# Performance work log

Hardware: AMD Instinct MI355X
Metric: run time of the kernel (lower is better)

Reference implementation:

```python
import jax, jax.numpy as jnp
import numpy as np

B, S, D = 4, 4096, 256


def setup_inputs() -> dict:
    key = jax.random.key(0)
    k1, k2, k3 = jax.random.split(key, 3)
    x = jax.random.normal(k1, (B, S, D), dtype=jnp.float32)
    w_int = jax.random.randint(k2, (D, D), 0, 127, dtype=jnp.int32)  # quantized weight (out, in)
    scale = jax.random.uniform(k3, (D,), dtype=jnp.float32)          # per-output-channel scale
    return {"x": x, "w_int": w_int, "scale": scale}


def reference(x, w_int, scale):
    # self-attention: q = k = v = x, single head over feature dim D
    inv_sqrt_d = 1.0 / jnp.sqrt(jnp.asarray(D, dtype=x.dtype))
    scores = jnp.einsum('bqd,bkd->bqk', x, x) * inv_sqrt_d   # [B,S,S]
    probs = jax.nn.softmax(scores, axis=-1)
    attn = jnp.einsum('bqk,bkd->bqd', probs, x)              # [B,S,D]
    # quantized linear: dequantize then matmul (y = attn @ W^T)
    W = w_int.astype(x.dtype) * scale[:, None]               # [D_out, D_in]
    return jnp.einsum('bsd,od->bso', attn, W)
```

## Files before the change

### kernel.cpp

```cpp
#include <hip/hip_runtime.h>

typedef __bf16 bf16x8 __attribute__((ext_vector_type(8)));
typedef float f32x16 __attribute__((ext_vector_type(16)));
typedef unsigned short u16x8 __attribute__((ext_vector_type(8)));

constexpr int B = 4, S = 4096, D = 256;
constexpr float CSC = 0.09016844005556021f;

static __device__ __forceinline__ unsigned short f2bf(float f) {
  unsigned int u = __builtin_bit_cast(unsigned int, f);
  u = (u + 0x7fffu + ((u >> 16) & 1u)) >> 16;
  return (unsigned short)u;
}

static __device__ __forceinline__ float bf2f(unsigned short u) {
  unsigned int v = ((unsigned int)u) << 16;
  return __builtin_bit_cast(float, v);
}

static __device__ __forceinline__ unsigned int pk2bf(float lo, float hi) {
  unsigned int r;
  asm("v_cvt_pk_bf16_f32 %0, %1, %2" : "=v"(r) : "v"(lo), "v"(hi));
  return r;
}

static __device__ __forceinline__ void gld16(const void* g, void* l) {
  __builtin_amdgcn_global_load_lds(
      (const __attribute__((address_space(1))) unsigned int*)g,
      (__attribute__((address_space(3))) unsigned int*)l, 16, 0, 0);
}

#define FENCE_ALL()                                               \
  do {                                                            \
    asm volatile("s_waitcnt vmcnt(0) lgkmcnt(0)" ::: "memory");   \
    __builtin_amdgcn_s_barrier();                                 \
    asm volatile("" ::: "memory");                                \
  } while (0)

__global__ __launch_bounds__(256) void k_prep(const float* __restrict__ x,
                                              unsigned short* __restrict__ xbf,
                                              unsigned short* __restrict__ xK,
                                              unsigned short* __restrict__ xV) {
  __shared__ unsigned short T[64][72];
  __shared__ unsigned short R[64][72];
  int bid = blockIdx.x;
  int b = bid >> 8, rem = bid & 255;
  int s0 = (rem >> 2) * 64, d0 = (rem & 3) * 64;
  int j = threadIdx.x & 63, i0 = threadIdx.x >> 6;
#pragma unroll
  for (int k = 0; k < 16; ++k) {
    int i = k * 4 + i0;
    int idx = (b * S + s0 + i) * D + d0 + j;
    unsigned short v = f2bf(x[idx]);
    xbf[idx] = v;
    T[j][i] = v;
    R[i][j] = v;
  }
  __syncthreads();
  int t = s0 >> 6;
#pragma unroll
  for (int p = 0; p < 2; ++p) {
    int cc = p * 256 + threadIdx.x;
    int i = cc >> 3;
    int sl = (cc >> 1) & 3;
    int half = cc & 1;
    u16x8 v = *(const u16x8*)&R[i][sl * 16 + half * 8];
    int s = (d0 >> 4) + sl;
    *(u16x8*)((char*)xK + (size_t)((b * 64 + t) * 16 + s) * 2048 + i * 32 + half * 16) = v;
  }
#pragma unroll
  for (int p = 0; p < 2; ++p) {
    int cc = p * 256 + threadIdx.x;
    int dl = cc >> 3;
    int p8 = cc & 7;
    u16x8 v = *(const u16x8*)&T[dl][p8 * 8];
    int c = p8 >> 1;
    *(u16x8*)((char*)xV + (size_t)((b * 64 + t) * 4 + c) * 8192 + (d0 + dl) * 32 +
              (p8 & 1) * 16) = v;
  }
}

__global__ __launch_bounds__(256) void k_deqw(const int* __restrict__ w,
                                              unsigned short* __restrict__ wbf) {
  int i = blockIdx.x * 256 + threadIdx.x;
  wbf[i] = f2bf((float)w[i]);
}

__global__ __launch_bounds__(512, 2) void k_attn(const unsigned short* __restrict__ xbf,
                                                 const unsigned short* __restrict__ xK,
                                                 const unsigned short* __restrict__ xV,
                                                 unsigned short* __restrict__ PO0,
                                                 unsigned short* __restrict__ PO1,
                                                 float* __restrict__ ML) {
  __shared__ __align__(16) char smem[132096];

  int tid = threadIdx.x;
  int w = tid >> 6, lane = tid & 63;
  int q5 = lane & 31, hi = lane >> 5;
  int pair = w >> 1, dh = w & 1;

  int bid = blockIdx.x;
  int swz = (bid & 7) * 32 + (bid >> 3);
  int h = swz & 1;
  int qg = swz >> 1;
  int q0 = qg * 128;
  int bat = q0 >> 12;
  int qloc = q0 & (S - 1);

  const unsigned short* Xb = xbf + (size_t)bat * (S * D);
  int qw = qloc + pair * 32;
  int koff = q5 * 32 + hi * 16;

  bf16x8 qf[16];
#pragma unroll
  for (int s = 0; s < 16; ++s)
    qf[s] = *(const bf16x8*)(Xb + (qw + q5) * D + s * 16 + hi * 8);

  f32x16 acc[8];
#pragma unroll
  for (int dt = 0; dt < 8; ++dt)
#pragma unroll
    for (int j = 0; j < 16; ++j) acc[dt][j] = 0.f;
  float l_lane = 0.f;

  const char* xKb = (const char*)xK + (size_t)(bat * 64 + h * 32) * 32768;
  const char* xVb = (const char*)xV + (size_t)(bat * 64 + h * 32) * 32768;

  auto STAGE = [&](int itile, int bb) {
    char* Kd = smem + bb * 32768;
    char* Vd = smem + 65536 + bb * 32768;
    const char* srcK = xKb + (size_t)itile * 32768;
    const char* srcV = xVb + (size_t)itile * 32768;
#pragma unroll
    for (int i = 0; i < 4; ++i) {
      int off = (w * 2 + (i >> 1)) * 2048 + (i & 1) * 1024;
      gld16(srcK + off + lane * 16, Kd + off);
    }
#pragma unroll
    for (int i = 0; i < 4; ++i) {
      int off = (w >> 1) * 8192 + ((w & 1) * 4 + i) * 1024;
      gld16(srcV + off + lane * 16, Vd + off);
    }
  };

  STAGE(0, 0);
  FENCE_ALL();

  for (int it = 0; it < 32; ++it) {
    int bb = it & 1;
    if (it + 1 < 32) STAGE(it + 1, bb ^ 1);

    const char* Kt = smem + bb * 32768 + dh * 1024 + koff;
    f32x16 st;
#pragma unroll
    for (int j = 0; j < 16; ++j) st[j] = 0.f;
    __builtin_amdgcn_s_setprio(1);
#pragma unroll
    for (int s = 0; s < 16; ++s) {
      bf16x8 kf = *(const bf16x8*)(Kt + s * 2048);
      st = __builtin_amdgcn_mfma_f32_32x32x16_bf16(kf, qf[s], st, 0, 0, 0);
    }
    __builtin_amdgcn_s_setprio(0);

    unsigned int pk[8];
    float ps = 0.f;
#pragma unroll
    for (int a = 0; a < 8; ++a) {
      float lo = exp2f(st[2 * a] * CSC);
      float hh = exp2f(st[2 * a + 1] * CSC);
      ps += lo + hh;
      pk[a] = pk2bf(lo, hh);
    }
    l_lane += ps;

    unsigned int a0 = pk[0], b0 = pk[2];
    unsigned int a1 = pk[1], b1 = pk[3];
    unsigned int a2 = pk[4], b2 = pk[6];
    unsigned int a3 = pk[5], b3 = pk[7];
    asm volatile("v_permlane32_swap_b32 %0, %1" : "+v"(a0), "+v"(b0));
    asm volatile("v_permlane32_swap_b32 %0, %1" : "+v"(a1), "+v"(b1));
    asm volatile("v_permlane32_swap_b32 %0, %1" : "+v"(a2), "+v"(b2));
    asm volatile("v_permlane32_swap_b32 %0, %1" : "+v"(a3), "+v"(b3));
    union PA { unsigned int u[4]; bf16x8 v; };
    PA pa0, pa1;
    pa0.u[0] = a0; pa0.u[1] = a1; pa0.u[2] = b0; pa0.u[3] = b1;
    pa1.u[0] = a2; pa1.u[1] = a3; pa1.u[2] = b2; pa1.u[3] = b3;

    __builtin_amdgcn_s_setprio(1);
#pragma unroll
    for (int s2i = 0; s2i < 2; ++s2i) {
      const char* Vt = smem + 65536 + bb * 32768 + (dh * 2 + s2i) * 8192 + koff;
      bf16x8 pa = (s2i == 0) ? pa0.v : pa1.v;
#pragma unroll
      for (int dt = 0; dt < 8; ++dt) {
        bf16x8 vf = *(const bf16x8*)(Vt + dt * 1024);
        acc[dt] = __builtin_amdgcn_mfma_f32_32x32x16_bf16(vf, pa, acc[dt], 0, 0, 0);
      }
    }
    __builtin_amdgcn_s_setprio(0);

    FENCE_ALL();
  }

  float lw = l_lane + __shfl_xor(l_lane, 32, 64);
  float* LX = (float*)(smem + 131072);
  if (lane < 32) LX[w * 32 + q5] = lw;
  __syncthreads();
  float l_tot = lw + LX[(w ^ 1) * 32 + q5];
  if (dh == 0 && lane < 32) {
    int row = q0 + pair * 32 + q5;
    ML[((size_t)h * 16384 + row) * 2 + 0] = 0.f;
    ML[((size_t)h * 16384 + row) * 2 + 1] = l_tot;
  }
  __syncthreads();

  unsigned short* Pb2 = (h == 0) ? PO0 : PO1;
#pragma unroll
  for (int rh = 0; rh < 2; ++rh) {
    float* slot = (float*)(smem + w * 16384);
#pragma unroll
    for (int dt4 = 0; dt4 < 4; ++dt4) {
#pragma unroll
      for (int r = 0; r < 16; ++r) {
        int dloc = dt4 * 32 + (r & 3) + 8 * (r >> 2) + 4 * hi;
        slot[dloc * 32 + q5] = acc[rh * 4 + dt4][r];
      }
    }
    __syncthreads();
    if (dh == rh) {
      const float* pslot = (const float*)(smem + (w ^ 1) * 16384);
#pragma unroll
      for (int dt4 = 0; dt4 < 4; ++dt4) {
#pragma unroll
        for (int r = 0; r < 16; ++r) {
          int dloc = dt4 * 32 + (r & 3) + 8 * (r >> 2) + 4 * hi;
          acc[rh * 4 + dt4][r] += pslot[dloc * 32 + q5];
        }
      }
      char* E = smem + w * 16384;
#pragma unroll
      for (int dt4 = 0; dt4 < 4; ++dt4) {
#pragma unroll
        for (int a = 0; a < 4; ++a) {
          int dl = dt4 * 32 + 8 * a + 4 * hi;
          *(unsigned int*)(E + q5 * 272 + dl * 2) =
              pk2bf(acc[rh * 4 + dt4][4 * a + 0], acc[rh * 4 + dt4][4 * a + 1]);
          *(unsigned int*)(E + q5 * 272 + dl * 2 + 4) =
              pk2bf(acc[rh * 4 + dt4][4 * a + 2], acc[rh * 4 + dt4][4 * a + 3]);
        }
      }
      asm volatile("s_waitcnt lgkmcnt(0)" ::: "memory");
#pragma unroll
      for (int i = 0; i < 8; ++i) {
        int qr = i * 4 + (lane >> 4);
        int ch = lane & 15;
        u16x8 v = *(const u16x8*)(E + qr * 272 + ch * 16);
        *(u16x8*)(Pb2 + (size_t)(q0 + pair * 32 + qr) * 256 + rh * 128 + ch * 8) = v;
      }
    }
    __syncthreads();
  }
}

__global__ __launch_bounds__(64) void k_gemm(const unsigned short* __restrict__ PO0,
                                             const unsigned short* __restrict__ PO1,
                                             const float* __restrict__ ML,
                                             const unsigned short* __restrict__ wbf,
                                             const float* __restrict__ scale,
                                             float* __restrict__ out) {
  int lane = threadIdx.x, g = lane >> 4, c = lane & 15;
  int m0 = blockIdx.x * 16;
  int o0 = blockIdx.y * 64;
  int row = m0 + c;
  float il = 1.f / (ML[(size_t)row * 2 + 1] + ML[((size_t)16384 + row) * 2 + 1]);
  union UU { uint4 u; bf16x8 v; };
  bf16x8 af[8];
#pragma unroll
  for (int dk = 0; dk < 8; ++dk) {
    u16x8 a0 = *(const u16x8*)(PO0 + (size_t)row * 256 + dk * 32 + g * 8);
    u16x8 a1 = *(const u16x8*)(PO1 + (size_t)row * 256 + dk * 32 + g * 8);
    UU cv;
#pragma unroll
    for (int e = 0; e < 4; ++e) {
      float lo = (bf2f(a0[2 * e]) + bf2f(a1[2 * e])) * il;
      float hi = (bf2f(a0[2 * e + 1]) + bf2f(a1[2 * e + 1])) * il;
      ((unsigned int*)&cv.u)[e] = pk2bf(lo, hi);
    }
    af[dk] = cv.v;
  }
  typedef float f32x4 __attribute__((ext_vector_type(4)));
  const f32x4 zero = {0.f, 0.f, 0.f, 0.f};
  f32x4 acc[4];
#pragma unroll
  for (int i = 0; i < 4; ++i) acc[i] = zero;
#pragma unroll
  for (int oc = 0; oc < 4; ++oc) {
#pragma unroll
    for (int dk = 0; dk < 8; ++dk) {
      bf16x8 wf = *(const bf16x8*)(wbf + (o0 + oc * 16 + c) * D + dk * 32 + g * 8);
      acc[oc] = __builtin_amdgcn_mfma_f32_16x16x32_bf16(af[dk], wf, acc[oc], 0, 0, 0);
    }
  }
#pragma unroll
  for (int oc = 0; oc < 4; ++oc) {
    float sc = scale[o0 + oc * 16 + c];
#pragma unroll
    for (int r = 0; r < 4; ++r)
      out[(m0 + 4 * g + r) * D + o0 + oc * 16 + c] = acc[oc][r] * sc;
  }
}

extern "C" void kernel_launch(void* const* d_in, const int* in_sizes, int n_in,
                              void* d_out, int out_size, void* d_ws, size_t ws_size,
                              hipStream_t stream) {
  (void)in_sizes; (void)n_in; (void)out_size; (void)ws_size;
  const float* x = (const float*)d_in[0];
  const int* w_int = (const int*)d_in[1];
  const float* scale = (const float*)d_in[2];
  float* out = (float*)d_out;

  char* ws = (char*)d_ws;
  unsigned short* xbf = (unsigned short*)(ws);
  unsigned short* xK  = (unsigned short*)(ws + 8388608);
  unsigned short* xV  = (unsigned short*)(ws + 16777216);
  unsigned short* wbf = (unsigned short*)(ws + 25165824);
  float*          ML  = (float*)(ws + 25296896);
  unsigned short* PO0 = (unsigned short*)(ws + 25821184);
  unsigned short* PO1 = (unsigned short*)(ws + 34209792);

  k_prep<<<dim3(1024), dim3(256), 0, stream>>>(x, xbf, xK, xV);
  k_deqw<<<dim3(256), dim3(256), 0, stream>>>(w_int, wbf);
  k_attn<<<dim3(256), dim3(512), 0, stream>>>(xbf, xK, xV, PO0, PO1, ML);
  k_gemm<<<dim3(1024, 4), dim3(64), 0, stream>>>(PO0, PO1, ML, wbf, scale, out);
}
```

Before: 116.7 us.

## Split QK MFMA chain into two accumulators and restructure output GEMM with LDS weights

In the attention kernel, the QK^T MFMA chain is split into two independent accumulators that are summed afterwards, which shortens the serial dependency between consecutive MFMAs. The output projection is rewritten so each 512-thread block handles 64 rows. It stages the whole bf16 weight matrix in LDS, in a layout pre-arranged by the dequant kernel, and uses 32x32x16 MFMAs. This replaces the 4096 tiny 64-thread blocks that reread weights from global memory, at the cost of 128KB of LDS per block and more vector registers.

```diff
diff --git a/kernel.cpp b/kernel.cpp
--- a/kernel.cpp
+++ b/kernel.cpp
@@ -81,9 +81,10 @@
 }
 
 __global__ __launch_bounds__(256) void k_deqw(const int* __restrict__ w,
-                                              unsigned short* __restrict__ wbf) {
-  int i = blockIdx.x * 256 + threadIdx.x;
-  wbf[i] = f2bf((float)w[i]);
+                                              unsigned short* __restrict__ wK) {
+  int o = blockIdx.x, d = threadIdx.x;
+  unsigned short v = f2bf((float)w[o * 256 + d]);
+  wK[(d >> 4) * 4096 + o * 16 + (d & 15)] = v;
 }
 
 __global__ __launch_bounds__(512, 2) void k_attn(const unsigned short* __restrict__ xbf,
@@ -151,16 +152,19 @@
     if (it + 1 < 32) STAGE(it + 1, bb ^ 1);
 
     const char* Kt = smem + bb * 32768 + dh * 1024 + koff;
-    f32x16 st;
-#pragma unroll
-    for (int j = 0; j < 16; ++j) st[j] = 0.f;
+    f32x16 sa, sb;
+#pragma unroll
+    for (int j = 0; j < 16; ++j) { sa[j] = 0.f; sb[j] = 0.f; }
     __builtin_amdgcn_s_setprio(1);
 #pragma unroll
-    for (int s = 0; s < 16; ++s) {
-      bf16x8 kf = *(const bf16x8*)(Kt + s * 2048);
-      st = __builtin_amdgcn_mfma_f32_32x32x16_bf16(kf, qf[s], st, 0, 0, 0);
+    for (int s = 0; s < 16; s += 2) {
+      bf16x8 kfa = *(const bf16x8*)(Kt + s * 2048);
+      bf16x8 kfb = *(const bf16x8*)(Kt + (s + 1) * 2048);
+      sa = __builtin_amdgcn_mfma_f32_32x32x16_bf16(kfa, qf[s], sa, 0, 0, 0);
+      sb = __builtin_amdgcn_mfma_f32_32x32x16_bf16(kfb, qf[s + 1], sb, 0, 0, 0);
     }
     __builtin_amdgcn_s_setprio(0);
+    f32x16 st = sa + sb;
 
     unsigned int pk[8];
     float ps = 0.f;
@@ -262,51 +266,71 @@
   }
 }
 
-__global__ __launch_bounds__(64) void k_gemm(const unsigned short* __restrict__ PO0,
-                                             const unsigned short* __restrict__ PO1,
-                                             const float* __restrict__ ML,
-                                             const unsigned short* __restrict__ wbf,
-                                             const float* __restrict__ scale,
-                                             float* __restrict__ out) {
-  int lane = threadIdx.x, g = lane >> 4, c = lane & 15;
-  int m0 = blockIdx.x * 16;
-  int o0 = blockIdx.y * 64;
-  int row = m0 + c;
+__global__ __launch_bounds__(512, 2) void k_gemm(const unsigned short* __restrict__ PO0,
+                                                 const unsigned short* __restrict__ PO1,
+                                                 const float* __restrict__ ML,
+                                                 const unsigned short* __restrict__ wK,
+                                                 const float* __restrict__ scale,
+                                                 float* __restrict__ out) {
+  __shared__ __align__(16) char Wl[131072];
+  int tid = threadIdx.x;
+  int w = tid >> 6, lane = tid & 63;
+  int q5 = lane & 31, hi = lane >> 5;
+  int msub = w & 1, oq = w >> 1;
+  int m0 = blockIdx.x * 64;
+
+#pragma unroll
+  for (int i = 0; i < 16; ++i) {
+    int off = (i * 512 + tid) * 16;
+    gld16((const char*)wK + off, Wl + off);
+  }
+
+  int row = m0 + msub * 32 + q5;
   float il = 1.f / (ML[(size_t)row * 2 + 1] + ML[((size_t)16384 + row) * 2 + 1]);
-  union UU { uint4 u; bf16x8 v; };
-  bf16x8 af[8];
-#pragma unroll
-  for (int dk = 0; dk < 8; ++dk) {
-    u16x8 a0 = *(const u16x8*)(PO0 + (size_t)row * 256 + dk * 32 + g * 8);
-    u16x8 a1 = *(const u16x8*)(PO1 + (size_t)row * 256 + dk * 32 + g * 8);
-    UU cv;
+
+  bf16x8 af[16];
+#pragma unroll
+  for (int s = 0; s < 16; ++s) {
+    u16x8 a0 = *(const u16x8*)(PO0 + (size_t)row * 256 + s * 16 + hi * 8);
+    u16x8 a1 = *(const u16x8*)(PO1 + (size_t)row * 256 + s * 16 + hi * 8);
+    union { unsigned int u[4]; bf16x8 v; } cv;
 #pragma unroll
     for (int e = 0; e < 4; ++e) {
       float lo = (bf2f(a0[2 * e]) + bf2f(a1[2 * e])) * il;
-      float hi = (bf2f(a0[2 * e + 1]) + bf2f(a1[2 * e + 1])) * il;
-      ((unsigned int*)&cv.u)[e] = pk2bf(lo, hi);
-    }
-    af[dk] = cv.v;
-  }
-  typedef float f32x4 __attribute__((ext_vector_type(4)));
-  const f32x4 zero = {0.f, 0.f, 0.f, 0.f};
-  f32x4 acc[4];
-#pragma unroll
-  for (int i = 0; i < 4; ++i) acc[i] = zero;
-#pragma unroll
-  for (int oc = 0; oc < 4; ++oc) {
-#pragma unroll
-    for (int dk = 0; dk < 8; ++dk) {
-      bf16x8 wf = *(const bf16x8*)(wbf + (o0 + oc * 16 + c) * D + dk * 32 + g * 8);
-      acc[oc] = __builtin_amdgcn_mfma_f32_16x16x32_bf16(af[dk], wf, acc[oc], 0, 0, 0);
-    }
-  }
-#pragma unroll
-  for (int oc = 0; oc < 4; ++oc) {
-    float sc = scale[o0 + oc * 16 + c];
-#pragma unroll
-    for (int r = 0; r < 4; ++r)
-      out[(m0 + 4 * g + r) * D + o0 + oc * 16 + c] = acc[oc][r] * sc;
+      float hh = (bf2f(a0[2 * e + 1]) + bf2f(a1[2 * e + 1])) * il;
+      cv.u[e] = pk2bf(lo, hh);
+    }
+    af[s] = cv.v;
+  }
+
+  asm volatile("s_waitcnt vmcnt(0)" ::: "memory");
+  __builtin_amdgcn_s_barrier();
+
+  f32x16 acc[2];
+#pragma unroll
+  for (int t = 0; t < 2; ++t)
+#pragma unroll
+    for (int j = 0; j < 16; ++j) acc[t][j] = 0.f;
+
+#pragma unroll
+  for (int t = 0; t < 2; ++t) {
+    int obase = (oq * 2 + t) * 32;
+#pragma unroll
+    for (int s = 0; s < 16; ++s) {
+      bf16x8 wf = *(const bf16x8*)(Wl + s * 8192 + (obase + q5) * 32 + hi * 16);
+      acc[t] = __builtin_amdgcn_mfma_f32_32x32x16_bf16(af[s], wf, acc[t], 0, 0, 0);
+    }
+  }
+
+#pragma unroll
+  for (int t = 0; t < 2; ++t) {
+    int o = (oq * 2 + t) * 32 + q5;
+    float sc = scale[o];
+#pragma unroll
+    for (int r = 0; r < 16; ++r) {
+      int mr = m0 + msub * 32 + (r & 3) + 8 * (r >> 2) + 4 * hi;
+      out[(size_t)mr * 256 + o] = acc[t][r] * sc;
+    }
   }
 }
 
@@ -323,13 +347,13 @@
   unsigned short* xbf = (unsigned short*)(ws);
   unsigned short* xK  = (unsigned short*)(ws + 8388608);
   unsigned short* xV  = (unsigned short*)(ws + 16777216);
-  unsigned short* wbf = (unsigned short*)(ws + 25165824);
+  unsigned short* wK  = (unsigned short*)(ws + 25165824);
   float*          ML  = (float*)(ws + 25296896);
   unsigned short* PO0 = (unsigned short*)(ws + 25821184);
   unsigned short* PO1 = (unsigned short*)(ws + 34209792);
 
   k_prep<<<dim3(1024), dim3(256), 0, stream>>>(x, xbf, xK, xV);
-  k_deqw<<<dim3(256), dim3(256), 0, stream>>>(w_int, wbf);
+  k_deqw<<<dim3(256), dim3(256), 0, stream>>>(w_int, wK);
   k_attn<<<dim3(256), dim3(512), 0, stream>>>(xbf, xK, xV, PO0, PO1, ML);
-  k_gemm<<<dim3(1024, 4), dim3(64), 0, stream>>>(PO0, PO1, ML, wbf, scale, out);
-}
+  k_gemm<<<dim3(256), dim3(512), 0, stream>>>(PO0, PO1, ML, wK, scale, out);
+}
```

Result: faster. 106.4 us (-8.9%).
